# Performance work log

Measured on AMD Instinct MI355X. Metric: run time of the kernel, lower is better.

## Reference

```python
import jax, jax.numpy as jnp
import numpy as np

THRESHOLD = 0.9  # module buffer _threshold (starting_threshold)


def setup_inputs() -> dict:
    key = jax.random.key(0)
    k_x, k_w = jax.random.split(key)
    B, T, D = 64, 577, 768
    x = jax.random.normal(k_x, (B, T, D), dtype=jnp.float32)
    # nn.Linear(in_dim, 1): weight [1, D] -> stored as vector [D], bias [1]
    w = jax.random.normal(k_w, (D,), dtype=jnp.float32) * (1.0 / np.sqrt(D))
    b = jnp.zeros((1,), dtype=jnp.float32)
    return {"x": x, "w": w, "b": b}


def reference(x, w, b):
    B, T, D = x.shape
    density = int(T * THRESHOLD)  # static: int(577*0.9) = 519
    # head: Linear(D,1) -> sigmoid -> [B, T]  (dropout is identity in eval)
    prob = jax.nn.sigmoid(jnp.einsum('btd,d->bt', x, w) + b[0])
    # keep top-`density` tokens by score (sorted descending, like torch.topk)
    _, top_idx = jax.lax.top_k(prob, density)
    tokens = jnp.take_along_axis(x, top_idx[..., None], axis=1)  # [B, density, D]
    # bottom (T - density) tokens: topk(largest=False) == topk of -prob,
    # which yields values sorted ascending in prob, matching torch
    n_skip = T - density  # 58 > 0
    neg_vals, skip_idx = jax.lax.top_k(-prob, n_skip)
    skip_tokens = jnp.take_along_axis(x, skip_idx[..., None], axis=1)  # [B, n_skip, D]
    weights = jax.nn.softmax(-neg_vals, axis=-1)  # softmax over skipped probs
    summary_token = jnp.sum(skip_tokens * weights[..., None], axis=1, keepdims=True)  # [B,1,D]
    return tokens, skip_tokens, summary_token
```

## Files before the change

kernel.cpp:

```cpp
#include <hip/hip_runtime.h>
#include <math.h>

#define BB 64
#define TT 577
#define DD 768
#define DENS 519
#define NSKIP 58
#define NROWS (BB * TT)

typedef float vf4 __attribute__((ext_vector_type(4)));

__device__ inline unsigned long long key_of(double z) {
    long long b = __double_as_longlong(z);
    return (b < 0) ? ~(unsigned long long)b
                   : ((unsigned long long)b | 0x8000000000000000ULL);
}
__device__ inline double key_inv(unsigned long long k) {
    long long b = (k >> 63) ? (long long)(k & 0x7fffffffffffffffULL)
                            : ~(long long)k;
    return __longlong_as_double(b);
}

__global__ __launch_bounds__(256) void k_prob(const float* __restrict__ x,
                                              const float* __restrict__ w,
                                              const float* __restrict__ bias,
                                              unsigned long long* __restrict__ keys) {
    int wave = (int)((blockIdx.x * blockDim.x + threadIdx.x) >> 6);
    int lane = threadIdx.x & 63;
    if (wave >= NROWS) return;
    const float4* r4 = (const float4*)(x + (size_t)wave * DD);
    const float4* w4 = (const float4*)w;
    double acc = 0.0;
#pragma unroll
    for (int i = 0; i < 3; ++i) {
        float4 a = r4[lane + 64 * i];
        float4 b = w4[lane + 64 * i];
        acc += (double)a.x * (double)b.x + (double)a.y * (double)b.y
             + (double)a.z * (double)b.z + (double)a.w * (double)b.w;
    }
#pragma unroll
    for (int off = 32; off; off >>= 1)
        acc += __shfl_down(acc, off, 64);
    if (lane == 0) keys[wave] = key_of(acc + (double)bias[0]);
}

__global__ __launch_bounds__(1024) void k_map(const float* __restrict__ x,
                                              const unsigned long long* __restrict__ keysG,
                                              int* __restrict__ dstRow,
                                              float* __restrict__ out) {
    __shared__ unsigned long long key[TT];
    __shared__ int   skipIdx[NSKIP];
    __shared__ float wsh[NSKIP];
    const int b   = blockIdx.x;
    const int tid = threadIdx.x;
    const float* xb = x + (size_t)b * TT * DD;

    if (tid < TT) key[tid] = keysG[b * TT + tid];
    __syncthreads();

    if (tid < TT) {
        const unsigned long long ki = key[tid];
        int rd = 0;
#pragma unroll 8
        for (int j = 0; j < TT; ++j) {
            unsigned long long kj = key[j];
            rd += ((kj > ki) | ((kj == ki) & (j < tid))) ? 1 : 0;
        }
        int dst;
        if (rd < DENS) {
            dst = b * DENS + rd;
        } else {
            int ra = (TT - 1) - rd;
            dst = BB * DENS + b * NSKIP + ra;
            skipIdx[ra] = tid;
        }
        dstRow[b * TT + tid] = dst;
    }
    __syncthreads();

    if (tid < 64) {
        double pv = -1.0e300;
        if (tid < NSKIP) {
            double z = key_inv(key[skipIdx[tid]]);
            pv = 1.0 / (1.0 + exp(-z));
        }
        double m = pv;
#pragma unroll
        for (int off = 32; off; off >>= 1) {
            double o = __shfl_down(m, off, 64);
            m = (o > m) ? o : m;
        }
        m = __shfl(m, 0, 64);
        double e = (tid < NSKIP) ? exp(pv - m) : 0.0;
        double s = e;
#pragma unroll
        for (int off = 32; off; off >>= 1)
            s += __shfl_down(s, off, 64);
        s = __shfl(s, 0, 64);
        if (tid < NSKIP) wsh[tid] = (float)(e / s);
    }
    __syncthreads();

    if (tid < DD) {
        float acc = 0.f;
#pragma unroll
        for (int k = 0; k < NSKIP; ++k)
            acc += wsh[k] * xb[(size_t)skipIdx[k] * DD + tid];
        out[(size_t)NROWS * DD + (size_t)b * DD + tid] = acc;
    }
}

__global__ __launch_bounds__(256) void k_copy(const float* __restrict__ x,
                                              const int* __restrict__ dstRow,
                                              float* __restrict__ out) {
    int wave = (int)((blockIdx.x * blockDim.x + threadIdx.x) >> 6);
    int lane = threadIdx.x & 63;
    if (wave >= NROWS) return;
    int dst = dstRow[wave];
    const vf4* s4 = (const vf4*)(x + (size_t)wave * DD);
    vf4* d4 = (vf4*)(out + (size_t)dst * DD);
#pragma unroll
    for (int c = 0; c < 3; ++c) {
        vf4 v = s4[lane + 64 * c];
        __builtin_nontemporal_store(v, &d4[lane + 64 * c]);
    }
}

extern "C" void kernel_launch(void* const* d_in, const int* in_sizes, int n_in,
                              void* d_out, int out_size, void* d_ws, size_t ws_size,
                              hipStream_t stream) {
    const float* x    = (const float*)d_in[0];
    const float* w    = (const float*)d_in[1];
    const float* bias = (const float*)d_in[2];
    float* out = (float*)d_out;
    char* ws = (char*)d_ws;

    unsigned long long* keys = (unsigned long long*)ws;
    int* dstRow = (int*)(ws + 295424);

    k_prob<<<NROWS / 4, 256, 0, stream>>>(x, w, bias, keys);
    k_map<<<BB, 1024, 0, stream>>>(x, keys, dstRow, out);
    k_copy<<<NROWS / 4, 256, 0, stream>>>(x, dstRow, out);
}
```

Baseline: 235.4 us.

## Fuse rank mapping and row copy into one scatter kernel with per-wave ranking

Merges the per-batch rank/summary kernel and the row-copy kernel into a single launch. The first BB blocks compute skip indices, softmax weights and the summary token. The remaining blocks each give one wave per row, which computes that row's rank itself with a wave-parallel comparison and reduction and then copies the row. This drops the dstRow workspace round trip, one kernel launch, and the serialization between the small 64-block map kernel and the copy. The cost is that every row's rank is recomputed redundantly, with each wave reading all 577 keys of its batch.

```diff
diff --git a/kernel.cpp b/kernel.cpp
--- a/kernel.cpp
+++ b/kernel.cpp
@@ -44,85 +44,97 @@
     if (lane == 0) keys[wave] = key_of(acc + (double)bias[0]);
 }
 
-__global__ __launch_bounds__(1024) void k_map(const float* __restrict__ x,
-                                              const unsigned long long* __restrict__ keysG,
-                                              int* __restrict__ dstRow,
-                                              float* __restrict__ out) {
+__global__ __launch_bounds__(256) void k_scatter(const float* __restrict__ x,
+                                                 const unsigned long long* __restrict__ keys,
+                                                 float* __restrict__ out) {
     __shared__ unsigned long long key[TT];
     __shared__ int   skipIdx[NSKIP];
     __shared__ float wsh[NSKIP];
-    const int b   = blockIdx.x;
+    const int blk = blockIdx.x;
     const int tid = threadIdx.x;
-    const float* xb = x + (size_t)b * TT * DD;
 
-    if (tid < TT) key[tid] = keysG[b * TT + tid];
-    __syncthreads();
-
-    if (tid < TT) {
-        const unsigned long long ki = key[tid];
+    if (blk < BB) {
+        const int b = blk;
+        const float* xb = x + (size_t)b * TT * DD;
+        for (int t = tid; t < TT; t += 256) key[t] = keys[b * TT + t];
+        __syncthreads();
+        for (int t = tid; t < TT; t += 256) {
+            const unsigned long long ki = key[t];
+            int rd = 0;
+#pragma unroll 8
+            for (int j = 0; j < TT; ++j) {
+                unsigned long long kj = key[j];
+                rd += ((kj > ki) | ((kj == ki) & (j < t))) ? 1 : 0;
+            }
+            if (rd >= DENS) skipIdx[(TT - 1) - rd] = t;
+        }
+        __syncthreads();
+        if (tid < 64) {
+            double pv = -1.0e300;
+            if (tid < NSKIP) {
+                double z = key_inv(key[skipIdx[tid]]);
+                pv = 1.0 / (1.0 + exp(-z));
+            }
+            double m = pv;
+#pragma unroll
+            for (int off = 32; off; off >>= 1) {
+                double o = __shfl_down(m, off, 64);
+                m = (o > m) ? o : m;
+            }
+            m = __shfl(m, 0, 64);
+            double e = (tid < NSKIP) ? exp(pv - m) : 0.0;
+            double s = e;
+#pragma unroll
+            for (int off = 32; off; off >>= 1)
+                s += __shfl_down(s, off, 64);
+            s = __shfl(s, 0, 64);
+            if (tid < NSKIP) wsh[tid] = (float)(e / s);
+        }
+        __syncthreads();
+        float a0 = 0.f, a1 = 0.f, a2 = 0.f;
+#pragma unroll
+        for (int k = 0; k < NSKIP; ++k) {
+            float wk = wsh[k];
+            const float* row = xb + (size_t)skipIdx[k] * DD;
+            a0 += wk * row[tid];
+            a1 += wk * row[tid + 256];
+            a2 += wk * row[tid + 512];
+        }
+        float* so = out + (size_t)NROWS * DD + (size_t)b * DD;
+        so[tid]       = a0;
+        so[tid + 256] = a1;
+        so[tid + 512] = a2;
+    } else {
+        int wave = (blk - BB) * 4 + (tid >> 6);
+        int lane = tid & 63;
+        int b = wave / TT;
+        int i = wave - b * TT;
+        const unsigned long long* kb = keys + b * TT;
+        unsigned long long ki = kb[i];
         int rd = 0;
-#pragma unroll 8
-        for (int j = 0; j < TT; ++j) {
-            unsigned long long kj = key[j];
-            rd += ((kj > ki) | ((kj == ki) & (j < tid))) ? 1 : 0;
+#pragma unroll
+        for (int c = 0; c < 10; ++c) {
+            int j = lane + 64 * c;
+            if (j < TT) {
+                unsigned long long kj = kb[j];
+                rd += ((kj > ki) | ((kj == ki) & (j < i))) ? 1 : 0;
+            }
         }
-        int dst;
-        if (rd < DENS) {
-            dst = b * DENS + rd;
-        } else {
-            int ra = (TT - 1) - rd;
-            dst = BB * DENS + b * NSKIP + ra;
-            skipIdx[ra] = tid;
-        }
-        dstRow[b * TT + tid] = dst;
-    }
-    __syncthreads();
-
-    if (tid < 64) {
-        double pv = -1.0e300;
-        if (tid < NSKIP) {
-            double z = key_inv(key[skipIdx[tid]]);
-            pv = 1.0 / (1.0 + exp(-z));
-        }
-        double m = pv;
-#pragma unroll
-        for (int off = 32; off; off >>= 1) {
-            double o = __shfl_down(m, off, 64);
-            m = (o > m) ? o : m;
-        }
-        m = __shfl(m, 0, 64);
-        double e = (tid < NSKIP) ? exp(pv - m) : 0.0;
-        double s = e;
 #pragma unroll
         for (int off = 32; off; off >>= 1)
-            s += __shfl_down(s, off, 64);
-        s = __shfl(s, 0, 64);
-        if (tid < NSKIP) wsh[tid] = (float)(e / s);
-    }
-    __syncthreads();
+            rd += __shfl_xor(rd, off, 64);
 
-    if (tid < DD) {
-        float acc = 0.f;
+        size_t dst = (rd < DENS)
+            ? (size_t)(b * DENS + rd) * DD
+            : (size_t)BB * DENS * DD + (size_t)(b * NSKIP + (TT - 1 - rd)) * DD;
+
+        const vf4* s4 = (const vf4*)(x + (size_t)wave * DD);
+        vf4* d4 = (vf4*)(out + dst);
 #pragma unroll
-        for (int k = 0; k < NSKIP; ++k)
-            acc += wsh[k] * xb[(size_t)skipIdx[k] * DD + tid];
-        out[(size_t)NROWS * DD + (size_t)b * DD + tid] = acc;
-    }
-}
-
-__global__ __launch_bounds__(256) void k_copy(const float* __restrict__ x,
-                                              const int* __restrict__ dstRow,
-                                              float* __restrict__ out) {
-    int wave = (int)((blockIdx.x * blockDim.x + threadIdx.x) >> 6);
-    int lane = threadIdx.x & 63;
-    if (wave >= NROWS) return;
-    int dst = dstRow[wave];
-    const vf4* s4 = (const vf4*)(x + (size_t)wave * DD);
-    vf4* d4 = (vf4*)(out + (size_t)dst * DD);
-#pragma unroll
-    for (int c = 0; c < 3; ++c) {
-        vf4 v = s4[lane + 64 * c];
-        __builtin_nontemporal_store(v, &d4[lane + 64 * c]);
+        for (int c = 0; c < 3; ++c) {
+            vf4 v = s4[lane + 64 * c];
+            __builtin_nontemporal_store(v, &d4[lane + 64 * c]);
+        }
     }
 }
 
@@ -133,12 +145,8 @@
     const float* w    = (const float*)d_in[1];
     const float* bias = (const float*)d_in[2];
     float* out = (float*)d_out;
-    char* ws = (char*)d_ws;
-
-    unsigned long long* keys = (unsigned long long*)ws;
-    int* dstRow = (int*)(ws + 295424);
+    unsigned long long* keys = (unsigned long long*)d_ws;
 
     k_prob<<<NROWS / 4, 256, 0, stream>>>(x, w, bias, keys);
-    k_map<<<BB, 1024, 0, stream>>>(x, keys, dstRow, out);
-    k_copy<<<NROWS / 4, 256, 0, stream>>>(x, dstRow, out);
+    k_scatter<<<BB + NROWS / 4, 256, 0, stream>>>(x, keys, out);
 }
```

Result: no change. 237.6 us (+0.9%).
